# Kernel tuning notes

Hardware: AMD Instinct MI355X
Metric: run time of the kernel (lower is better)

Reference implementation:

```python
import jax, jax.numpy as jnp
import numpy as np

B, C, H, W = 8, 512, 48, 48
WSCALE = 0.02  # keep pre-softmax energies in a sane range


def _conv(x, w, b, stride, pad):
    y = jax.lax.conv_general_dilated(
        x, w, (stride, stride), [(pad, pad), (pad, pad)],
        dimension_numbers=("NCHW", "OIHW", "NCHW"))
    return y + b[None, :, None, None]


def setup_inputs() -> dict:
    key = jax.random.key(0)
    ks = jax.random.split(key, 9)
    return {
        "x": jax.random.normal(ks[0], (B, C, H, W), jnp.float32),
        "Wqc": jax.random.normal(ks[1], (2 * C, C, 3, 3), jnp.float32) * WSCALE,
        "bqc": jax.random.normal(ks[2], (2 * C,), jnp.float32) * WSCALE,
        "Wkc": jax.random.normal(ks[3], (C, C, 3, 3), jnp.float32) * WSCALE,
        "bkc": jax.random.normal(ks[4], (C,), jnp.float32) * WSCALE,
        "Wqp": jax.random.normal(ks[5], (C // 8, C, 1, 1), jnp.float32) * WSCALE,
        "bqp": jax.random.normal(ks[6], (C // 8,), jnp.float32) * WSCALE,
        "Wkp": jax.random.normal(ks[7], (C // 8, C, 1, 1), jnp.float32) * WSCALE,
        "bkp": jax.random.normal(ks[8], (C // 8,), jnp.float32) * WSCALE,
    }


def reference(x, Wqc, bqc, Wkc, bkc, Wqp, bqp, Wkp, bkp):
    b, c, h, w = x.shape
    hw = h * w
    # --- channel attention (CAM) on stride-2 downsampled q/k ---
    qc = _conv(x, Wqc, bqc, 2, 1).reshape(b, 2 * c, -1)   # (B, 2C, H'W')
    kc = _conv(x, Wkc, bkc, 2, 1).reshape(b, c, -1)       # (B, C,  H'W')
    energy = jnp.einsum("bqm,bcm->bqc", qc, kc)            # (B, 2C, C)
    # max-subtraction trick from the source: max - energy, then softmax
    energy_new = jnp.max(energy, axis=-1, keepdims=True) - energy
    attn_c = jax.nn.softmax(energy_new, axis=-1)
    xf = x.reshape(b, c, hw)
    out_c = jnp.einsum("bqc,bcn->bqn", attn_c, xf)         # (B, 2C, HW)
    # --- position attention (PAM) ---
    qp = _conv(x, Wqp, bqp, 1, 0).reshape(b, c // 8, hw)   # (B, C/8, HW)
    kp = _conv(x, Wkp, bkp, 1, 0).reshape(b, c // 8, hw)   # (B, C/8, HW)
    energy_p = jnp.einsum("bdn,bdm->bnm", qp, kp)          # (B, HW, HW)
    attn_p = jax.nn.softmax(energy_p, axis=-1)
    # out_c @ attn_p^T
    out_p = jnp.einsum("bqn,bmn->bqm", out_c, attn_p)      # (B, 2C, HW)
    return out_c, out_p.reshape(b, 2 * c, h, w)
```

## Files before the change

### kernel.cpp

```cpp
#include <hip/hip_runtime.h>
#include <hip/hip_bf16.h>

typedef unsigned short u16;
typedef __attribute__((ext_vector_type(8))) _Float16 half8;
typedef __attribute__((ext_vector_type(4))) float f32x4;

static __device__ __forceinline__ u16 f2h(float v) {
  return __builtin_bit_cast(u16, (_Float16)v);
}
static __device__ __forceinline__ float h2f(u16 u) {
  return (float)__builtin_bit_cast(_Float16, u);
}

static __device__ __forceinline__ void gll16(const void* g, void* l) {
  __builtin_amdgcn_global_load_lds(
      (const __attribute__((address_space(1))) unsigned int*)g,
      (__attribute__((address_space(3))) unsigned int*)l, 16, 0, 0);
}

template <bool ASPLIT, bool BSPLIT, int EPI>
__global__ __launch_bounds__(256) void gemm_bt(
    const u16* __restrict__ A, const u16* __restrict__ Al,
    const u16* __restrict__ B, const u16* __restrict__ Bl,
    float* __restrict__ Cf, u16* __restrict__ Ch, u16* __restrict__ Cl,
    const float* __restrict__ bias0, const float* __restrict__ bias1,
    int biasSplit, int K, int lda, int ldb, int ldc,
    long long sA, long long sB, long long sC) {
  __shared__ __align__(16) u16 smA[2][(ASPLIT ? 2 : 1) * 128 * 32];
  __shared__ __align__(16) u16 smB[2][(BSPLIT ? 2 : 1) * 128 * 32];

  const int tid = threadIdx.x;
  const int wave = tid >> 6, lane = tid & 63;
  const int wr = wave >> 1, wc = wave & 1;
  const long long z = blockIdx.z;
  A += z * sA;
  B += z * sB;
  if (ASPLIT) Al += z * sA;
  if (BSPLIT) Bl += z * sB;
  const long long tM = (long long)blockIdx.y * 128;
  const long long tN = (long long)blockIdx.x * 128;
  const int r4 = lane >> 2, kc = lane & 3;

  const long long arow0 = (tM + wave * 16 + r4) * (long long)lda + kc * 8;
  const long long arow1 = arow0 + 64LL * lda;
  const long long brow0 = (tN + wave * 16 + r4) * (long long)ldb + kc * 8;
  const long long brow1 = brow0 + 64LL * ldb;

  auto stage = [&](int bf, long long ko) {
    u16* dA = &smA[bf][wave * 512];
    u16* dB = &smB[bf][wave * 512];
    gll16(A + arow0 + ko, dA);
    gll16(A + arow1 + ko, dA + 2048);
    gll16(B + brow0 + ko, dB);
    gll16(B + brow1 + ko, dB + 2048);
    if constexpr (ASPLIT) {
      gll16(Al + arow0 + ko, dA + 4096);
      gll16(Al + arow1 + ko, dA + 4096 + 2048);
    }
    if constexpr (BSPLIT) {
      gll16(Bl + brow0 + ko, dB + 4096);
      gll16(Bl + brow1 + ko, dB + 4096 + 2048);
    }
  };

  f32x4 acc[4][4];
#pragma unroll
  for (int i = 0; i < 4; i++)
#pragma unroll
    for (int j = 0; j < 4; j++) acc[i][j] = f32x4{0.f, 0.f, 0.f, 0.f};

  const int quad = lane >> 4, mr = lane & 15;
  const int nk = K >> 5;

  stage(0, 0);

  for (int kt = 0; kt < nk; ++kt) {
    const int cur = kt & 1;
    asm volatile("s_waitcnt vmcnt(0)" ::: "memory");
    __builtin_amdgcn_s_barrier();
    asm volatile("" ::: "memory");

    half8 a[4], b[4];
#pragma unroll
    for (int i = 0; i < 4; i++)
      a[i] = *(const half8*)&smA[cur][(wr * 64 + i * 16 + mr) * 32 + quad * 8];
#pragma unroll
    for (int j = 0; j < 4; j++)
      b[j] = *(const half8*)&smB[cur][(wc * 64 + j * 16 + mr) * 32 + quad * 8];

    if (kt + 1 < nk) stage(cur ^ 1, (long long)(kt + 1) * 32);

#pragma unroll
    for (int i = 0; i < 4; i++)
#pragma unroll
      for (int j = 0; j < 4; j++)
        acc[i][j] = __builtin_amdgcn_mfma_f32_16x16x32_f16(a[i], b[j], acc[i][j], 0, 0, 0);

    if constexpr (ASPLIT) {
      half8 al[4];
#pragma unroll
      for (int i = 0; i < 4; i++)
        al[i] = *(const half8*)&smA[cur][4096 + (wr * 64 + i * 16 + mr) * 32 + quad * 8];
#pragma unroll
      for (int i = 0; i < 4; i++)
#pragma unroll
        for (int j = 0; j < 4; j++)
          acc[i][j] = __builtin_amdgcn_mfma_f32_16x16x32_f16(al[i], b[j], acc[i][j], 0, 0, 0);
    }
    if constexpr (BSPLIT) {
      half8 bl[4];
#pragma unroll
      for (int j = 0; j < 4; j++)
        bl[j] = *(const half8*)&smB[cur][4096 + (wc * 64 + j * 16 + mr) * 32 + quad * 8];
#pragma unroll
      for (int i = 0; i < 4; i++)
#pragma unroll
        for (int j = 0; j < 4; j++)
          acc[i][j] = __builtin_amdgcn_mfma_f32_16x16x32_f16(a[i], bl[j], acc[i][j], 0, 0, 0);
    }
  }

#pragma unroll
  for (int i = 0; i < 4; i++) {
#pragma unroll
    for (int j = 0; j < 4; j++) {
      const long long gn = tN + wc * 64 + j * 16 + mr;
#pragma unroll
      for (int p = 0; p < 4; p++) {
        const long long gm = tM + wr * 64 + i * 16 + quad * 4 + p;
        float v = acc[i][j][p];
        if constexpr (EPI == 1) v += (gm < biasSplit) ? bias0[gm] : bias1[gm - biasSplit];
        if constexpr (EPI == 3) v += (gn < biasSplit) ? bias0[gn] : bias1[gn - biasSplit];
        const long long off = z * sC + gm * ldc + gn;
        if constexpr (EPI == 0) {
          Cf[off] = v;
        } else if constexpr (EPI == 1) {
          u16 h = f2h(v);
          Ch[off] = h;
          Cl[off] = f2h(v - h2f(h));
        } else if constexpr (EPI == 2) {
          Cf[off] = v;
          Ch[off] = f2h(v);
        } else {
          Ch[off] = f2h(v);
        }
      }
    }
  }
  (void)biasSplit;
}

__global__ void im2col_kernel(const float* __restrict__ x, u16* __restrict__ Ph) {
  int idx = blockIdx.x * 256 + threadIdx.x;
  int k = idx % 4608;
  int m = idx / 4608;
  int kx = k % 3, t = k / 3;
  int ky = t % 3, c = t / 3;
  int ox = m % 24, t2 = m / 24;
  int oy = t2 % 24, b = t2 / 24;
  int ix = 2 * ox - 1 + kx, iy = 2 * oy - 1 + ky;
  float v = 0.f;
  if (ix >= 0 && ix < 48 && iy >= 0 && iy < 48)
    v = x[((b * 512 + c) * 48 + iy) * 48 + ix];
  Ph[idx] = f2h(v);
}

__global__ void wprep_kernel(const float* __restrict__ Wqc, const float* __restrict__ Wkc,
                             u16* __restrict__ Wh, u16* __restrict__ Wl) {
  int idx = blockIdx.x * 256 + threadIdx.x;
  int n = idx / 4608;
  float v = (n < 1024) ? Wqc[idx] : Wkc[idx - 1024 * 4608];
  u16 h = f2h(v);
  Wh[idx] = h;
  Wl[idx] = f2h(v - h2f(h));
}

__global__ void wp_prep(const float* __restrict__ Wqp, const float* __restrict__ Wkp,
                        u16* __restrict__ Wp) {
  int idx = blockIdx.x * 256 + threadIdx.x;
  int d = idx >> 9;
  float v = (d < 64) ? Wqp[idx] : Wkp[idx - 64 * 512];
  Wp[idx] = f2h(v);
}

__global__ void xt_kernel(const float* __restrict__ x, u16* __restrict__ xt) {
  __shared__ float t[32][33];
  int b = blockIdx.z;
  int sp0 = blockIdx.x * 32, c0 = blockIdx.y * 32;
  int tx = threadIdx.x & 31, ty = threadIdx.x >> 5;
#pragma unroll
  for (int k = 0; k < 4; k++) {
    int c = c0 + ty + k * 8;
    t[ty + k * 8][tx] = x[((long long)(b * 512 + c)) * 2304 + sp0 + tx];
  }
  __syncthreads();
#pragma unroll
  for (int k = 0; k < 4; k++) {
    int sp = sp0 + ty + k * 8;
    xt[((long long)b * 2304 + sp) * 512 + c0 + tx] = f2h(t[tx][ty + k * 8]);
  }
}

__global__ void softmax_cam(const float* __restrict__ E, u16* __restrict__ attn) {
  __shared__ float sm[4];
  const long long r = blockIdx.x;
  const float* e = E + r * 512;
  int tid = threadIdx.x, wave = tid >> 6, lane = tid & 63;
  float v0 = e[tid], v1 = e[tid + 256];
  float mn = fminf(v0, v1);
#pragma unroll
  for (int o = 32; o; o >>= 1) mn = fminf(mn, __shfl_xor(mn, o));
  if (lane == 0) sm[wave] = mn;
  __syncthreads();
  mn = fminf(fminf(sm[0], sm[1]), fminf(sm[2], sm[3]));
  float p0 = __expf(mn - v0), p1 = __expf(mn - v1);
  float s = p0 + p1;
#pragma unroll
  for (int o = 32; o; o >>= 1) s += __shfl_xor(s, o);
  __syncthreads();
  if (lane == 0) sm[wave] = s;
  __syncthreads();
  float inv = 1.f / (sm[0] + sm[1] + sm[2] + sm[3]);
  attn[r * 512 + tid] = f2h(p0 * inv);
  attn[r * 512 + tid + 256] = f2h(p1 * inv);
}

__global__ void softmax_pam(u16* __restrict__ EP) {
  __shared__ float sm[4];
  const long long r = blockIdx.x;
  u16* e = EP + r * 2304;
  int tid = threadIdx.x, wave = tid >> 6, lane = tid & 63;
  float v[9];
#pragma unroll
  for (int k = 0; k < 9; k++) v[k] = h2f(e[tid + 256 * k]);
  float mx = v[0];
#pragma unroll
  for (int k = 1; k < 9; k++) mx = fmaxf(mx, v[k]);
#pragma unroll
  for (int o = 32; o; o >>= 1) mx = fmaxf(mx, __shfl_xor(mx, o));
  if (lane == 0) sm[wave] = mx;
  __syncthreads();
  mx = fmaxf(fmaxf(sm[0], sm[1]), fmaxf(sm[2], sm[3]));
  float s = 0.f;
#pragma unroll
  for (int k = 0; k < 9; k++) {
    v[k] = __expf(v[k] - mx);
    s += v[k];
  }
#pragma unroll
  for (int o = 32; o; o >>= 1) s += __shfl_xor(s, o);
  __syncthreads();
  if (lane == 0) sm[wave] = s;
  __syncthreads();
  float inv = 1.f / (sm[0] + sm[1] + sm[2] + sm[3]);
#pragma unroll
  for (int k = 0; k < 9; k++) e[tid + 256 * k] = f2h(v[k] * inv);
}

extern "C" void kernel_launch(void* const* d_in, const int* in_sizes, int n_in,
                              void* d_out, int out_size, void* d_ws, size_t ws_size,
                              hipStream_t stream) {
  const float* x   = (const float*)d_in[0];
  const float* Wqc = (const float*)d_in[1];
  const float* bqc = (const float*)d_in[2];
  const float* Wkc = (const float*)d_in[3];
  const float* bkc = (const float*)d_in[4];
  const float* Wqp = (const float*)d_in[5];
  const float* bqp = (const float*)d_in[6];
  const float* Wkp = (const float*)d_in[7];
  const float* bkp = (const float*)d_in[8];
  float* outc = (float*)d_out;
  float* outp = outc + 8LL * 1024 * 2304;

  if (ws_size < 195166208ULL) return;

  char* ws = (char*)d_ws;
  u16*   P    = (u16*)(ws + 0);
  u16*   Wh   = (u16*)(ws + 42467328LL);
  u16*   Wl   = (u16*)(ws + 56623104LL);
  u16*   EP   = (u16*)(ws + 0);
  u16*   qcth = (u16*)(ws + 84934656LL);
  u16*   qctl = (u16*)(ws + 99090432LL);
  u16*   pp   = (u16*)(ws + 84934656LL);
  float* E    = (float*)(ws + 113246208LL);
  u16*   attn = (u16*)(ws + 130023424LL);
  u16*   xt   = (u16*)(ws + 138412032LL);
  u16*   ocb  = (u16*)(ws + 157286400LL);
  u16*   Wp   = (u16*)(ws + 195035136LL);

  wprep_kernel<<<27648, 256, 0, stream>>>(Wqc, Wkc, Wh, Wl);
  wp_prep<<<256, 256, 0, stream>>>(Wqp, Wkp, Wp);
  im2col_kernel<<<82944, 256, 0, stream>>>(x, P);
  xt_kernel<<<dim3(72, 16, 8), 256, 0, stream>>>(x, xt);

  gemm_bt<true, false, 1><<<dim3(36, 12, 1), 256, 0, stream>>>(
      Wh, Wl, P, nullptr, nullptr, qcth, qctl, bqc, bkc, 1024,
      4608, 4608, 4608, 4608, 0, 0, 0);

  gemm_bt<true, true, 0><<<dim3(4, 8, 8), 256, 0, stream>>>(
      qcth, qctl, qcth + 1024LL * 4608, qctl + 1024LL * 4608,
      E, nullptr, nullptr,
      nullptr, nullptr, 0, 576, 4608, 4608, 512, 576, 576, 524288);

  softmax_cam<<<8192, 256, 0, stream>>>(E, attn);

  gemm_bt<false, false, 2><<<dim3(18, 8, 8), 256, 0, stream>>>(
      attn, nullptr, xt, nullptr, outc, ocb, nullptr,
      nullptr, nullptr, 0, 512, 512, 512, 2304, 524288, 1179648, 2359296);

  gemm_bt<false, false, 3><<<dim3(1, 144, 1), 256, 0, stream>>>(
      xt, nullptr, Wp, nullptr, nullptr, pp, nullptr,
      bqp, bkp, 64, 512, 512, 512, 128, 0, 0, 0);

  gemm_bt<false, false, 4><<<dim3(18, 18, 8), 256, 0, stream>>>(
      pp, nullptr, pp + 64, nullptr, nullptr, EP, nullptr,
      nullptr, nullptr, 0, 64, 128, 128, 2304, 294912, 294912, 5308416);

  softmax_pam<<<18432, 256, 0, stream>>>(EP);

  gemm_bt<false, false, 0><<<dim3(18, 8, 8), 256, 0, stream>>>(
      ocb, nullptr, EP, nullptr, outp, nullptr, nullptr,
      nullptr, nullptr, 0, 2304, 2304, 2304, 2304, 2359296, 5308416, 2359296);

  (void)in_sizes; (void)n_in; (void)out_size;
}
```

Before: 686.0 us.

## Triple-buffer GEMM LDS staging and remap workgroups across XCDs

```diff
diff --git a/kernel.cpp b/kernel.cpp
--- a/kernel.cpp
+++ b/kernel.cpp
@@ -16,6 +16,14 @@
   __builtin_amdgcn_global_load_lds(
       (const __attribute__((address_space(1))) unsigned int*)g,
       (__attribute__((address_space(3))) unsigned int*)l, 16, 0, 0);
+}
+
+template <int N>
+static __device__ __forceinline__ void wait_vm() {
+  if constexpr (N == 0) asm volatile("s_waitcnt vmcnt(0)" ::: "memory");
+  else if constexpr (N == 4) asm volatile("s_waitcnt vmcnt(4)" ::: "memory");
+  else if constexpr (N == 6) asm volatile("s_waitcnt vmcnt(6)" ::: "memory");
+  else asm volatile("s_waitcnt vmcnt(8)" ::: "memory");
 }
 
 template <bool ASPLIT, bool BSPLIT, int EPI>
@@ -26,19 +34,29 @@
     const float* __restrict__ bias0, const float* __restrict__ bias1,
     int biasSplit, int K, int lda, int ldb, int ldc,
     long long sA, long long sB, long long sC) {
-  __shared__ __align__(16) u16 smA[2][(ASPLIT ? 2 : 1) * 128 * 32];
-  __shared__ __align__(16) u16 smB[2][(BSPLIT ? 2 : 1) * 128 * 32];
+  __shared__ __align__(16) u16 smA[3][(ASPLIT ? 2 : 1) * 128 * 32];
+  __shared__ __align__(16) u16 smB[3][(BSPLIT ? 2 : 1) * 128 * 32];
+  constexpr int G = 4 + (ASPLIT ? 2 : 0) + (BSPLIT ? 2 : 0);
 
   const int tid = threadIdx.x;
   const int wave = tid >> 6, lane = tid & 63;
   const int wr = wave >> 1, wc = wave & 1;
-  const long long z = blockIdx.z;
+
+  const int gx = gridDim.x, gy = gridDim.y;
+  const int nwg = gx * gy * (int)gridDim.z;
+  const int bid = (int)blockIdx.x + gx * ((int)blockIdx.y + gy * (int)blockIdx.z);
+  const int w = (bid & 7) * (nwg >> 3) + (bid >> 3);
+  const int bx = w % gx;
+  const int rem = w / gx;
+  const int by = rem % gy;
+  const long long z = rem / gy;
+
   A += z * sA;
   B += z * sB;
   if (ASPLIT) Al += z * sA;
   if (BSPLIT) Bl += z * sB;
-  const long long tM = (long long)blockIdx.y * 128;
-  const long long tN = (long long)blockIdx.x * 128;
+  const long long tM = (long long)by * 128;
+  const long long tN = (long long)bx * 128;
   const int r4 = lane >> 2, kc = lane & 3;
 
   const long long arow0 = (tM + wave * 16 + r4) * (long long)lda + kc * 8;
@@ -73,10 +91,11 @@
   const int nk = K >> 5;
 
   stage(0, 0);
-
+  if (nk > 1) stage(1, 32);
+
+  int cur = 0;
   for (int kt = 0; kt < nk; ++kt) {
-    const int cur = kt & 1;
-    asm volatile("s_waitcnt vmcnt(0)" ::: "memory");
+    if (kt < nk - 1) wait_vm<G>(); else wait_vm<0>();
     __builtin_amdgcn_s_barrier();
     asm volatile("" ::: "memory");
 
@@ -88,7 +107,10 @@
     for (int j = 0; j < 4; j++)
       b[j] = *(const half8*)&smB[cur][(wc * 64 + j * 16 + mr) * 32 + quad * 8];
 
-    if (kt + 1 < nk) stage(cur ^ 1, (long long)(kt + 1) * 32);
+    if (kt + 2 < nk) {
+      int pf = cur + 2; if (pf >= 3) pf -= 3;
+      stage(pf, (long long)(kt + 2) * 32);
+    }
 
 #pragma unroll
     for (int i = 0; i < 4; i++)
@@ -118,6 +140,7 @@
         for (int j = 0; j < 4; j++)
           acc[i][j] = __builtin_amdgcn_mfma_f32_16x16x32_f16(a[i], bl[j], acc[i][j], 0, 0, 0);
     }
+    cur = (cur == 2) ? 0 : cur + 1;
   }
 
 #pragma unroll
```

Result: no change. 674.2 us (-1.7%).
